# Kernel optimization log

Hardware: AMD Instinct MI355X
Metric: run time of the kernel (lower is better)

## Reference

```python
import jax, jax.numpy as jnp
import numpy as np

S, B, N, F_IN = 15, 32, 3000, 16
NHID, GH = 2, 1
G_FEAT = GH * N          # 3000
R_FEAT = G_FEAT // 3     # 1000
H_RNN = 3
N_LAYERS = 2
OUT = 1
E = 48000
EPS = 1e-5


def setup_inputs() -> dict:
    key = jax.random.key(0)
    ks = jax.random.split(key, 24)
    r = lambda k, shp: (jax.random.normal(k, shp, jnp.float32) * 0.1)
    inp = {
        "x": jax.random.normal(ks[0], (S, B, N, F_IN), jnp.float32),
        "edge_index": jax.random.randint(ks[1], (2, E), 0, N, dtype=jnp.int32),
        # per-timestep GCN params (stacked over seq axis)
        "conv1_W": r(ks[2], (S, F_IN, NHID)),
        "conv1_b": r(ks[3], (S, NHID)),
        "conv2_W": r(ks[4], (S, NHID, GH)),
        "conv2_b": r(ks[5], (S, GH)),
        # per-timestep Linear(G_FEAT -> R_FEAT), stored (S, in, out)
        "lin_W": r(ks[6], (S, G_FEAT, R_FEAT)) * 0.1,
        "lin_b": r(ks[7], (S, R_FEAT)),
        # per-timestep BatchNorm1d(R_FEAT) affine params
        "bn_gamma": jnp.ones((S, R_FEAT), jnp.float32),
        "bn_beta": jnp.zeros((S, R_FEAT), jnp.float32),
        # 2-layer GRU: layer 0 (R_FEAT -> H_RNN), layer 1 (H_RNN -> H_RNN)
        "gru_Wih0": r(ks[8], (3 * H_RNN, R_FEAT)),
        "gru_Whh0": r(ks[9], (3 * H_RNN, H_RNN)),
        "gru_bih0": r(ks[10], (3 * H_RNN,)),
        "gru_bhh0": r(ks[11], (3 * H_RNN,)),
        "gru_Wih1": r(ks[12], (3 * H_RNN, H_RNN)),
        "gru_Whh1": r(ks[13], (3 * H_RNN, H_RNN)),
        "gru_bih1": r(ks[14], (3 * H_RNN,)),
        "gru_bhh1": r(ks[15], (3 * H_RNN,)),
        # decoder Linear(H_RNN -> OUT)
        "dec_W": r(ks[16], (H_RNN, OUT)),
        "dec_b": r(ks[17], (OUT,)),
    }
    return inp


def _gcn_norm(edge_index):
    """Add self loops and compute symmetric GCN normalization per edge."""
    loop = jnp.arange(N, dtype=edge_index.dtype)
    src = jnp.concatenate([edge_index[0], loop])
    dst = jnp.concatenate([edge_index[1], loop])
    deg = jax.ops.segment_sum(jnp.ones_like(src, jnp.float32), dst, num_segments=N)
    dinv = jax.lax.rsqrt(deg)  # deg >= 1 due to self loops
    norm = dinv[src] * dinv[dst]
    return src, dst, norm


def _gru_layer(xs, Wih, Whh, bih, bhh):
    H = Whh.shape[1]

    def step(h, xt):
        gi = xt @ Wih.T + bih
        gh = h @ Whh.T + bhh
        ir, iz, inn = jnp.split(gi, 3, axis=-1)
        hr, hz, hn = jnp.split(gh, 3, axis=-1)
        r = jax.nn.sigmoid(ir + hr)
        z = jax.nn.sigmoid(iz + hz)
        n = jnp.tanh(inn + r * hn)
        h_new = (1.0 - z) * n + z * h
        return h_new, h_new

    h0 = jnp.zeros((xs.shape[1], H), xs.dtype)
    hT, ys = jax.lax.scan(step, h0, xs)
    return ys, hT


def reference(x, edge_index, conv1_W, conv1_b, conv2_W, conv2_b, lin_W, lin_b,
              bn_gamma, bn_beta, gru_Wih0, gru_Whh0, gru_bih0, gru_bhh0,
              gru_Wih1, gru_Whh1, gru_bih1, gru_bhh1, dec_W, dec_b):
    src, dst, norm = _gcn_norm(edge_index)

    def gconv(h, W, b):
        # per-timestep weights: h (S,B,N,f), W (S,f,g)
        h = jnp.einsum('sbnf,sfg->sbng', h, W) + b[:, None, None, :]
        msg = h[:, :, src, :] * norm[None, None, :, None]
        out = jnp.zeros((S, B, N, W.shape[-1]), h.dtype)
        return out.at[:, :, dst, :].add(msg)

    g = jax.nn.sigmoid(gconv(x, conv1_W, conv1_b))      # dropout: eval mode (identity)
    g = jax.nn.sigmoid(gconv(g, conv2_W, conv2_b))      # (S,B,N,GH)
    g = g.reshape(S, B, G_FEAT)

    y = jnp.einsum('sbg,sgr->sbr', g, lin_W) + lin_b[:, None, :]
    # BatchNorm1d per timestep over the batch axis (training-mode batch stats)
    mu = jnp.mean(y, axis=1, keepdims=True)
    var = jnp.var(y, axis=1, keepdims=True)
    y = bn_gamma[:, None, :] * (y - mu) * jax.lax.rsqrt(var + EPS) + bn_beta[:, None, :]

    y1, h1 = _gru_layer(y, gru_Wih0, gru_Whh0, gru_bih0, gru_bhh0)
    y2, h2 = _gru_layer(y1, gru_Wih1, gru_Whh1, gru_bih1, gru_bhh1)
    hn = jnp.stack([h1, h2])                 # (n_layers, B, H_RNN)

    out = y2 @ dec_W + dec_b                 # (S, B, OUT)
    return out, hn
```

## Files before the change

kernel.cpp:

```cpp
#include <hip/hip_runtime.h>
#include <hip/hip_bf16.h>

#define S_ 15
#define B_ 32
#define N_ 3000
#define FIN 16
#define RF 1000
#define GEMM_NC 25
#define NCHK 120

__device__ __forceinline__ float sigf(float x){ return 1.0f/(1.0f+expf(-x)); }

__global__ void k_zero(int* p, int n){
  int i = blockIdx.x*blockDim.x + threadIdx.x;
  if (i < n) p[i] = 0;
}

__global__ void k_count(const int* __restrict__ dst, int E, int* __restrict__ cnt){
  int e = blockIdx.x*blockDim.x + threadIdx.x;
  if (e < E) atomicAdd(&cnt[dst[e]], 1);
}

__global__ void k_scan(const int* __restrict__ cnt, int* __restrict__ indptr,
                       int* __restrict__ cursor, float* __restrict__ dinv){
  __shared__ int sc[1024];
  int tid = threadIdx.x;
  int i0 = tid*3;
  int c0 = (i0+0 < N_) ? cnt[i0+0] : 0;
  int c1 = (i0+1 < N_) ? cnt[i0+1] : 0;
  int c2 = (i0+2 < N_) ? cnt[i0+2] : 0;
  int ssum = c0+c1+c2;
  sc[tid] = ssum; __syncthreads();
  for (int off=1; off<1024; off<<=1){
    int add = (tid>=off) ? sc[tid-off] : 0;
    __syncthreads();
    sc[tid] += add;
    __syncthreads();
  }
  int excl = sc[tid]-ssum;
  if (i0+0 < N_){ indptr[i0+0]=excl;       cursor[i0+0]=excl;       dinv[i0+0]=rsqrtf((float)(c0+1)); }
  if (i0+1 < N_){ indptr[i0+1]=excl+c0;    cursor[i0+1]=excl+c0;    dinv[i0+1]=rsqrtf((float)(c1+1)); }
  if (i0+2 < N_){ indptr[i0+2]=excl+c0+c1; cursor[i0+2]=excl+c0+c1; dinv[i0+2]=rsqrtf((float)(c2+1)); }
  if (tid==1023) indptr[N_] = sc[1023];
}

__global__ void k_fill(const int* __restrict__ src, const int* __restrict__ dst, int E,
                       int* __restrict__ cursor, const float* __restrict__ dinv,
                       int* __restrict__ col, float* __restrict__ wgt){
  int e = blockIdx.x*blockDim.x + threadIdx.x;
  if (e < E){
    int d = dst[e], s = src[e];
    int pos = atomicAdd(&cursor[d], 1);
    col[pos] = s;
    wgt[pos] = dinv[s]*dinv[d];
  }
}

__global__ __launch_bounds__(256) void k_t1(const float* __restrict__ x, const float* __restrict__ W1,
                     const float* __restrict__ b1, float2* __restrict__ t1){
  __shared__ float2 lds[64*33];
  int s = blockIdx.y;
  int n0 = blockIdx.x*64;
  int tid = threadIdx.x;
  const float* w = W1 + s*FIN*2;
  float wv[32];
  #pragma unroll
  for (int i=0; i<32; ++i) wv[i] = w[i];
  float bb0 = b1[s*2+0], bb1 = b1[s*2+1];
  int nl = tid & 63, q = tid >> 6;
  #pragma unroll
  for (int bi=0; bi<8; ++bi){
    int b = bi*4 + q;
    int n = n0 + nl;
    if (n < N_){
      const float4* xp = (const float4*)(x + ((size_t)(s*B_+b)*N_ + n)*FIN);
      float4 x0 = xp[0], x1 = xp[1], x2 = xp[2], x3 = xp[3];
      float xv[16] = {x0.x,x0.y,x0.z,x0.w, x1.x,x1.y,x1.z,x1.w,
                      x2.x,x2.y,x2.z,x2.w, x3.x,x3.y,x3.z,x3.w};
      float a0 = bb0, a1 = bb1;
      #pragma unroll
      for (int f=0; f<16; ++f){ a0 += xv[f]*wv[f*2+0]; a1 += xv[f]*wv[f*2+1]; }
      lds[nl*33 + b] = make_float2(a0, a1);
    }
  }
  __syncthreads();
  #pragma unroll
  for (int k=0; k<8; ++k){
    int n = k*8 + (tid>>5);
    int b = tid & 31;
    int gn = n0 + n;
    if (gn < N_) t1[(size_t)(s*N_+gn)*32 + b] = lds[n*33 + b];
  }
}

__global__ void k_conv1(const float* __restrict__ t1, const int* __restrict__ indptr,
                        const int* __restrict__ col, const float* __restrict__ wgt,
                        const float* __restrict__ dinv, const float* __restrict__ W2,
                        const float* __restrict__ b2, float* __restrict__ t2){
  int s = blockIdx.y;
  int wv = threadIdx.x >> 6, lane = threadIdx.x & 63;
  int bb = lane >> 1, k = lane & 1;
  float w20 = W2[s*2+0], w21 = W2[s*2+1], bias2 = b2[s];
  const float* tbase = t1 + (size_t)s*N_*64;
  int d0 = (blockIdx.x*4 + wv)*2;
  for (int i=0; i<2; ++i){
    int d = d0 + i;
    if (d >= N_) break;
    int ip0 = indptr[d], ip1 = indptr[d+1];
    float di = dinv[d];
    float acc0 = tbase[(size_t)d*64 + lane] * (di*di);
    float acc1 = 0.f, acc2 = 0.f, acc3 = 0.f;
    int e = ip0;
    for (; e+4 <= ip1; e += 4){
      int   c0 = col[e],  c1 = col[e+1],  c2 = col[e+2],  c3 = col[e+3];
      float f0 = wgt[e],  f1 = wgt[e+1],  f2 = wgt[e+2],  f3 = wgt[e+3];
      acc0 += f0 * tbase[(size_t)c0*64 + lane];
      acc1 += f1 * tbase[(size_t)c1*64 + lane];
      acc2 += f2 * tbase[(size_t)c2*64 + lane];
      acc3 += f3 * tbase[(size_t)c3*64 + lane];
    }
    for (; e < ip1; ++e)
      acc0 += wgt[e] * tbase[(size_t)col[e]*64 + lane];
    float gk = sigf((acc0+acc1)+(acc2+acc3));
    float other = __shfl_xor(gk, 1);
    if (k == 0) t2[(size_t)(s*N_+d)*32 + bb] = gk*w20 + other*w21 + bias2;
  }
}

__global__ void k_conv2(const float* __restrict__ t2, const int* __restrict__ indptr,
                        const int* __restrict__ col, const float* __restrict__ wgt,
                        const float* __restrict__ dinv, float* __restrict__ g){
  int s = blockIdx.y;
  int wv = threadIdx.x >> 6, lane = threadIdx.x & 63;
  int half = lane >> 5, bb = lane & 31;
  const float* tbase = t2 + (size_t)s*N_*32;
  int d = (blockIdx.x*4 + wv)*2 + half;
  if (d < N_){
    int ip0 = indptr[d], ip1 = indptr[d+1];
    float di = dinv[d];
    float acc0 = tbase[(size_t)d*32 + bb] * (di*di);
    float acc1 = 0.f, acc2 = 0.f, acc3 = 0.f;
    int e = ip0;
    for (; e+4 <= ip1; e += 4){
      int   c0 = col[e],  c1 = col[e+1],  c2 = col[e+2],  c3 = col[e+3];
      float f0 = wgt[e],  f1 = wgt[e+1],  f2 = wgt[e+2],  f3 = wgt[e+3];
      acc0 += f0 * tbase[(size_t)c0*32 + bb];
      acc1 += f1 * tbase[(size_t)c1*32 + bb];
      acc2 += f2 * tbase[(size_t)c2*32 + bb];
      acc3 += f3 * tbase[(size_t)c3*32 + bb];
    }
    for (; e < ip1; ++e)
      acc0 += wgt[e] * tbase[(size_t)col[e]*32 + bb];
    g[(size_t)(s*N_+d)*32 + bb] = sigf((acc0+acc1)+(acc2+acc3));
  }
}

__global__ __launch_bounds__(256) void k_gemm(const float* __restrict__ g,
                                              const float* __restrict__ W,
                                              float* __restrict__ partial){
  int s = blockIdx.z, c = blockIdx.y, r0 = blockIdx.x*256;
  int tid = threadIdx.x;
  int r = r0 + tid;
  bool act = r < RF;
  const float* gbase = g + (size_t)(s*N_ + c*NCHK)*32;
  const float* wp = W + (size_t)(s*N_ + c*NCHK)*RF + (act ? r : 0);
  float acc[32];
  #pragma unroll
  for (int i=0; i<32; ++i) acc[i] = 0.f;
  float wbuf[8];
  #pragma unroll
  for (int i=0; i<8; ++i) wbuf[i] = wp[(size_t)i*RF];
  for (int n0=0; n0<NCHK; n0+=8){
    float wcur[8];
    #pragma unroll
    for (int i=0; i<8; ++i) wcur[i] = wbuf[i];
    if (n0+8 < NCHK){
      const float* wn = wp + (size_t)(n0+8)*RF;
      #pragma unroll
      for (int i=0; i<8; ++i) wbuf[i] = wn[(size_t)i*RF];
    }
    #pragma unroll
    for (int i=0; i<8; ++i){
      const float* gb = gbase + (size_t)(n0+i)*32;
      float wv = wcur[i];
      #pragma unroll
      for (int b=0; b<32; ++b) acc[b] += gb[b]*wv;
    }
  }
  if (act){
    float4* pp = (float4*)(partial + (size_t)c*(S_*RF*32) + ((size_t)s*RF + r)*32);
    #pragma unroll
    for (int q=0; q<8; ++q)
      pp[q] = make_float4(acc[q*4+0], acc[q*4+1], acc[q*4+2], acc[q*4+3]);
  }
}

__global__ void k_redbn(const float* __restrict__ partial, const float* __restrict__ gamma,
                        const float* __restrict__ beta, float* __restrict__ y){
  int idx = blockIdx.x*256 + threadIdx.x;
  if (idx >= S_*RF*8) return;
  int sr = idx >> 3, b4 = idx & 7;
  const float4* p4 = (const float4*)partial;
  float4 v = make_float4(0.f,0.f,0.f,0.f);
  #pragma unroll
  for (int c=0; c<GEMM_NC; ++c){
    float4 t = p4[(size_t)c*(S_*RF*8) + (size_t)sr*8 + b4];
    v.x += t.x; v.y += t.y; v.z += t.z; v.w += t.w;
  }
  float s1 = (v.x+v.y) + (v.z+v.w);
  #pragma unroll
  for (int off=1; off<8; off<<=1) s1 += __shfl_xor(s1, off);
  float mu = s1 * (1.f/32.f);
  float dx = v.x-mu, dy = v.y-mu, dz = v.z-mu, dw = v.w-mu;
  float q = (dx*dx+dy*dy) + (dz*dz+dw*dw);
  #pragma unroll
  for (int off=1; off<8; off<<=1) q += __shfl_xor(q, off);
  float var = q * (1.f/32.f);
  float sc = gamma[sr]*rsqrtf(var + 1e-5f);
  float sh = beta[sr] - mu*sc;
  ((float4*)y)[(size_t)sr*8 + b4] =
      make_float4(v.x*sc+sh, v.y*sc+sh, v.z*sc+sh, v.w*sc+sh);
}

__global__ void k_gi0(const float* __restrict__ y, const float* __restrict__ Wih0,
                      float* __restrict__ gi0p){
  int s = blockIdx.x, rq = blockIdx.y;
  int tid = threadIdx.x;
  if (tid >= 288) return;
  int b = tid & 31, j = tid >> 5;
  const float* yb = y + (size_t)s*RF*32 + b;
  const float* wj = Wih0 + j*RF;
  float a = 0.f;
  int r0 = rq*250, r1 = r0 + 250;
  #pragma unroll 5
  for (int r=r0; r<r1; ++r) a += yb[(size_t)r*32] * wj[r];
  gi0p[((size_t)(s*32+b)*9 + j)*4 + rq] = a;
}

__global__ void k_gru(const float* __restrict__ gi0p, const float* __restrict__ Whh0,
                      const float* __restrict__ bhh0, const float* __restrict__ bih0,
                      const float* __restrict__ Wih1, const float* __restrict__ Whh1,
                      const float* __restrict__ bih1, const float* __restrict__ bhh1,
                      const float* __restrict__ dW, const float* __restrict__ db,
                      float* __restrict__ out){
  int b = threadIdx.x;
  if (b >= 32) return;
  float whh0[27], wih1[27], whh1[27], bh0[9], bi0[9], bi1[9], bh1[9];
  #pragma unroll
  for (int i=0; i<27; ++i){ whh0[i]=Whh0[i]; wih1[i]=Wih1[i]; whh1[i]=Whh1[i]; }
  #pragma unroll
  for (int i=0; i<9; ++i){ bh0[i]=bhh0[i]; bi0[i]=bih0[i]; bi1[i]=bih1[i]; bh1[i]=bhh1[i]; }
  float dw0=dW[0], dw1=dW[1], dw2=dW[2], db0=db[0];
  float h0[3]={0,0,0}, h1[3]={0,0,0}, nh[3];
  for (int t=0; t<S_; ++t){
    const float* gp = gi0p + (size_t)(t*32+b)*36;
    float gi[9], gh[9];
    #pragma unroll
    for (int j=0; j<9; ++j){
      gi[j] = ((gp[j*4+0]+gp[j*4+1]) + (gp[j*4+2]+gp[j*4+3])) + bi0[j];
      gh[j] = bh0[j] + whh0[j*3+0]*h0[0] + whh0[j*3+1]*h0[1] + whh0[j*3+2]*h0[2];
    }
    #pragma unroll
    for (int k=0; k<3; ++k){
      float r = sigf(gi[k]+gh[k]);
      float z = sigf(gi[3+k]+gh[3+k]);
      float nn = tanhf(gi[6+k] + r*gh[6+k]);
      nh[k] = (1.f-z)*nn + z*h0[k];
    }
    h0[0]=nh[0]; h0[1]=nh[1]; h0[2]=nh[2];
    float gi1[9], gh1[9];
    #pragma unroll
    for (int j=0; j<9; ++j){
      gi1[j] = bi1[j] + wih1[j*3+0]*h0[0] + wih1[j*3+1]*h0[1] + wih1[j*3+2]*h0[2];
      gh1[j] = bh1[j] + whh1[j*3+0]*h1[0] + whh1[j*3+1]*h1[1] + whh1[j*3+2]*h1[2];
    }
    #pragma unroll
    for (int k=0; k<3; ++k){
      float r = sigf(gi1[k]+gh1[k]);
      float z = sigf(gi1[3+k]+gh1[3+k]);
      float nn = tanhf(gi1[6+k] + r*gh1[6+k]);
      nh[k] = (1.f-z)*nn + z*h1[k];
    }
    h1[0]=nh[0]; h1[1]=nh[1]; h1[2]=nh[2];
    float o = dw0*h1[0] + dw1*h1[1] + dw2*h1[2] + db0;
    out[t*32 + b] = o;
  }
  #pragma unroll
  for (int j=0; j<3; ++j){
    out[S_*B_ + b*3 + j]        = h0[j];
    out[S_*B_ + 96 + b*3 + j]   = h1[j];
  }
}

extern "C" void kernel_launch(void* const* d_in, const int* in_sizes, int n_in,
                              void* d_out, int out_size, void* d_ws, size_t ws_size,
                              hipStream_t stream) {
  const float* x    = (const float*)d_in[0];
  const int*   ei   = (const int*)d_in[1];
  int E = in_sizes[1] / 2;
  const float* c1W  = (const float*)d_in[2];
  const float* c1b  = (const float*)d_in[3];
  const float* c2W  = (const float*)d_in[4];
  const float* c2b  = (const float*)d_in[5];
  const float* linW = (const float*)d_in[6];
  const float* gma  = (const float*)d_in[8];
  const float* bta  = (const float*)d_in[9];
  const float* Wih0 = (const float*)d_in[10];
  const float* Whh0 = (const float*)d_in[11];
  const float* bih0 = (const float*)d_in[12];
  const float* bhh0 = (const float*)d_in[13];
  const float* Wih1 = (const float*)d_in[14];
  const float* Whh1 = (const float*)d_in[15];
  const float* bih1 = (const float*)d_in[16];
  const float* bhh1 = (const float*)d_in[17];
  const float* dW   = (const float*)d_in[18];
  const float* db   = (const float*)d_in[19];

  char* ws = (char*)d_ws;
  size_t off = 0;
  auto take = [&](size_t bytes)->char* {
    char* p = ws + off;
    off = (off + bytes + 255) & ~(size_t)255;
    return p;
  };
  int*    cnt     = (int*)take(N_*4);
  int*    indptr  = (int*)take((N_+1)*4);
  int*    cursor  = (int*)take(N_*4);
  float*  dinv    = (float*)take(N_*4);
  int*    col     = (int*)take((size_t)E*4);
  float*  wgt     = (float*)take((size_t)E*4);
  float*  gi0p    = (float*)take((size_t)S_*B_*9*4*4);
  float2* t1      = (float2*)take((size_t)S_*N_*B_*8);
  float*  t2      = (float*)take((size_t)S_*N_*B_*4);
  float*  g       = (float*)take((size_t)S_*N_*B_*4);
  float*  y       = (float*)take((size_t)S_*B_*RF*4);
  float*  partial = (float*)take((size_t)GEMM_NC*S_*RF*32*4);

  const int* esrc = ei;
  const int* edst = ei + E;

  k_zero<<<(N_+255)/256, 256, 0, stream>>>(cnt, N_);
  k_count<<<(E+255)/256, 256, 0, stream>>>(edst, E, cnt);
  k_scan<<<1, 1024, 0, stream>>>(cnt, indptr, cursor, dinv);
  k_fill<<<(E+255)/256, 256, 0, stream>>>(esrc, edst, E, cursor, dinv, col, wgt);
  k_t1<<<dim3((N_+63)/64, S_), 256, 0, stream>>>(x, c1W, c1b, t1);
  k_conv1<<<dim3((N_+7)/8, S_), 256, 0, stream>>>((const float*)t1, indptr, col, wgt, dinv, c2W, c2b, t2);
  k_conv2<<<dim3((N_+7)/8, S_), 256, 0, stream>>>(t2, indptr, col, wgt, dinv, g);
  k_gemm<<<dim3(4, GEMM_NC, S_), 256, 0, stream>>>(g, linW, partial);
  k_redbn<<<(S_*RF*8+255)/256, 256, 0, stream>>>(partial, gma, bta, y);
  k_gi0<<<dim3(S_, 4), 320, 0, stream>>>(y, Wih0, gi0p);
  k_gru<<<1, 64, 0, stream>>>(gi0p, Whh0, bhh0, bih0, Wih1, Whh1, bih1, bhh1, dW, db,
                              (float*)d_out);
}
```

Baseline: 210.8 us.

## Fuse CSR fill with first GCN transform and prefetch GRU inputs

Merges the edge-fill kernel and the per-node first linear transform into one launch, splitting blocks by index, which removes a kernel launch and lets the two independent jobs overlap. Changes GEMM K-split from 25 to 15 chunks of 200, which cuts the partial-sum buffer and reduction work but gives the GEMM fewer blocks. The serial GRU kernel now loads the next timestep's gate inputs as float4 before computing the current step, hiding memory latency in the recurrence.

```diff
diff --git a/kernel.cpp b/kernel.cpp
--- a/kernel.cpp
+++ b/kernel.cpp
@@ -6,8 +6,8 @@
 #define N_ 3000
 #define FIN 16
 #define RF 1000
-#define GEMM_NC 25
-#define NCHK 120
+#define GEMM_NC 15
+#define NCHK 200
 
 __device__ __forceinline__ float sigf(float x){ return 1.0f/(1.0f+expf(-x)); }
 
@@ -44,23 +44,27 @@
   if (tid==1023) indptr[N_] = sc[1023];
 }
 
-__global__ void k_fill(const int* __restrict__ src, const int* __restrict__ dst, int E,
-                       int* __restrict__ cursor, const float* __restrict__ dinv,
-                       int* __restrict__ col, float* __restrict__ wgt){
-  int e = blockIdx.x*blockDim.x + threadIdx.x;
-  if (e < E){
-    int d = dst[e], s = src[e];
-    int pos = atomicAdd(&cursor[d], 1);
-    col[pos] = s;
-    wgt[pos] = dinv[s]*dinv[d];
-  }
-}
-
-__global__ __launch_bounds__(256) void k_t1(const float* __restrict__ x, const float* __restrict__ W1,
-                     const float* __restrict__ b1, float2* __restrict__ t1){
+__global__ __launch_bounds__(256) void k_fill_t1(
+    const int* __restrict__ src, const int* __restrict__ dst, int E, int fillB,
+    int* __restrict__ cursor, const float* __restrict__ dinv,
+    int* __restrict__ col, float* __restrict__ wgt,
+    const float* __restrict__ x, const float* __restrict__ W1,
+    const float* __restrict__ b1, float2* __restrict__ t1, int nt1x){
   __shared__ float2 lds[64*33];
-  int s = blockIdx.y;
-  int n0 = blockIdx.x*64;
+  int bid = blockIdx.x;
+  if (bid < fillB){
+    int e = bid*256 + threadIdx.x;
+    if (e < E){
+      int d = dst[e], s = src[e];
+      int pos = atomicAdd(&cursor[d], 1);
+      col[pos] = s;
+      wgt[pos] = dinv[s]*dinv[d];
+    }
+    return;
+  }
+  int b2 = bid - fillB;
+  int s  = b2 / nt1x;
+  int n0 = (b2 % nt1x)*64;
   int tid = threadIdx.x;
   const float* w = W1 + s*FIN*2;
   float wv[32];
@@ -252,12 +256,25 @@
   for (int i=0; i<9; ++i){ bh0[i]=bhh0[i]; bi0[i]=bih0[i]; bi1[i]=bih1[i]; bh1[i]=bhh1[i]; }
   float dw0=dW[0], dw1=dW[1], dw2=dW[2], db0=db[0];
   float h0[3]={0,0,0}, h1[3]={0,0,0}, nh[3];
+  const float4* gp4 = (const float4*)gi0p;
+  float4 nxt[9];
+  #pragma unroll
+  for (int qq=0; qq<9; ++qq) nxt[qq] = gp4[(size_t)b*9 + qq];
   for (int t=0; t<S_; ++t){
-    const float* gp = gi0p + (size_t)(t*32+b)*36;
+    float cur[36];
+    #pragma unroll
+    for (int qq=0; qq<9; ++qq){
+      cur[qq*4+0]=nxt[qq].x; cur[qq*4+1]=nxt[qq].y;
+      cur[qq*4+2]=nxt[qq].z; cur[qq*4+3]=nxt[qq].w;
+    }
+    if (t+1 < S_){
+      #pragma unroll
+      for (int qq=0; qq<9; ++qq) nxt[qq] = gp4[(size_t)((t+1)*32+b)*9 + qq];
+    }
     float gi[9], gh[9];
     #pragma unroll
     for (int j=0; j<9; ++j){
-      gi[j] = ((gp[j*4+0]+gp[j*4+1]) + (gp[j*4+2]+gp[j*4+3])) + bi0[j];
+      gi[j] = ((cur[j*4+0]+cur[j*4+1]) + (cur[j*4+2]+cur[j*4+3])) + bi0[j];
       gh[j] = bh0[j] + whh0[j*3+0]*h0[0] + whh0[j*3+1]*h0[1] + whh0[j*3+2]*h0[2];
     }
     #pragma unroll
@@ -339,11 +356,15 @@
   const int* esrc = ei;
   const int* edst = ei + E;
 
+  int fillB = (E + 255) / 256;
+  int nt1x  = (N_ + 63) / 64;
+
   k_zero<<<(N_+255)/256, 256, 0, stream>>>(cnt, N_);
   k_count<<<(E+255)/256, 256, 0, stream>>>(edst, E, cnt);
   k_scan<<<1, 1024, 0, stream>>>(cnt, indptr, cursor, dinv);
-  k_fill<<<(E+255)/256, 256, 0, stream>>>(esrc, edst, E, cursor, dinv, col, wgt);
-  k_t1<<<dim3((N_+63)/64, S_), 256, 0, stream>>>(x, c1W, c1b, t1);
+  k_fill_t1<<<fillB + nt1x*S_, 256, 0, stream>>>(esrc, edst, E, fillB,
+                                                 cursor, dinv, col, wgt,
+                                                 x, c1W, c1b, t1, nt1x);
   k_conv1<<<dim3((N_+7)/8, S_), 256, 0, stream>>>((const float*)t1, indptr, col, wgt, dinv, c2W, c2b, t2);
   k_conv2<<<dim3((N_+7)/8, S_), 256, 0, stream>>>(t2, indptr, col, wgt, dinv, g);
   k_gemm<<<dim3(4, GEMM_NC, S_), 256, 0, stream>>>(g, linW, partial);
```

New measurement: 215.6 us. 1.02x slower.
